# Optimization experiments

Hardware: AMD Instinct MI355X
Metric: run time of the kernel (lower is better)

Reference implementation:

```python
import jax, jax.numpy as jnp
import numpy as np

DIM = 1024
HEADS = 16
DIM_HEAD = 64
INNER = HEADS * DIM_HEAD  # 1024
EPS = 1e-5


def layer_norm(x, g, b):
    mu = jnp.mean(x, axis=-1, keepdims=True)
    var = jnp.var(x, axis=-1, keepdims=True)
    return (x - mu) * jax.lax.rsqrt(var + EPS) * g + b


def setup_inputs() -> dict:
    key = jax.random.key(0)
    ks = jax.random.split(key, 8)
    s = 0.02
    return {
        "x": jax.random.normal(ks[0], (2, 2048, DIM), dtype=jnp.float32),
        "w_qkv": jax.random.normal(ks[1], (DIM, 3 * INNER), dtype=jnp.float32) * s,
        "w_out": jax.random.normal(ks[2], (INNER, DIM), dtype=jnp.float32) * s,
        "b_out": jnp.zeros((DIM,), jnp.float32),
        "g1": jnp.ones((DIM,), jnp.float32),
        "bt1": jnp.zeros((DIM,), jnp.float32),
        "g2": jnp.ones((DIM,), jnp.float32),
        "bt2": jnp.zeros((DIM,), jnp.float32),
        "w1": jax.random.normal(ks[3], (DIM, DIM), dtype=jnp.float32) * s,  # ff hidden = dim_out = DIM
        "b1": jnp.zeros((DIM,), jnp.float32),
        "w2": jax.random.normal(ks[4], (DIM, DIM), dtype=jnp.float32) * s,
        "b2": jnp.zeros((DIM,), jnp.float32),
    }


def reference(x, w_qkv, w_out, b_out, g1, bt1, g2, bt2, w1, b1, w2, b2):
    b, n, _ = x.shape
    scale = DIM_HEAD ** (-0.5)
    x_in = x
    xl = layer_norm(x, g1, bt1)
    qkv = xl @ w_qkv  # [b, n, 3*inner]
    q, k, v = jnp.split(qkv, 3, axis=-1)
    def split_heads(t):
        return t.reshape(b, n, HEADS, DIM_HEAD).transpose(0, 2, 1, 3)  # b h n d
    q, k, v = map(split_heads, (q, k, v))
    dots = jnp.einsum('bhid,bhjd->bhij', q, k) * scale
    attn = jax.nn.softmax(dots, axis=-1)
    out = jnp.einsum('bhij,bhjd->bhid', attn, v)
    out = out.transpose(0, 2, 1, 3).reshape(b, n, INNER)
    out = out @ w_out + b_out
    out = out + x_in
    h = layer_norm(out, g2, bt2)
    h = jax.nn.gelu(h @ w1 + b1, approximate=False) @ w2 + b2
    return h + out
```

## Files before the change

kernel.cpp:

```cpp
#include <hip/hip_runtime.h>
#include <math.h>

typedef __attribute__((ext_vector_type(4))) float f32x4;
typedef __attribute__((ext_vector_type(8))) short bf16x8;
typedef __attribute__((ext_vector_type(8))) unsigned short u16x8;

#define DIM 1024
#define SEQ 2048
#define NHEADS 16
#define DH 64

__device__ __forceinline__ unsigned short f2bf(float f) {
    unsigned int u = __builtin_bit_cast(unsigned int, f);
    u += 0x7fffu + ((u >> 16) & 1u);
    return (unsigned short)(u >> 16);
}

__device__ __forceinline__ float bf2f(unsigned short s) {
    unsigned int u = (unsigned int)s << 16;
    return __builtin_bit_cast(float, u);
}

__device__ __forceinline__ unsigned int cvt_pk_bf16(float lo, float hi) {
    unsigned int r;
    asm("v_cvt_pk_bf16_f32 %0, %1, %2" : "=v"(r) : "v"(lo), "v"(hi));
    return r;
}

__device__ __forceinline__ float fexp2(float x) {
    float r;
    asm("v_exp_f32 %0, %1" : "=v"(r) : "v"(x));
    return r;
}

__device__ __forceinline__ void gld16(const unsigned short* g, unsigned short* l) {
    __builtin_amdgcn_global_load_lds((const __attribute__((address_space(1))) void*)g,
                                     (__attribute__((address_space(3))) void*)l, 16, 0, 0);
}

__global__ __launch_bounds__(256) void wtrans_ln(const float* __restrict__ wq,
                                                 const float* __restrict__ wo,
                                                 const float* __restrict__ wf1,
                                                 const float* __restrict__ wf2,
                                                 unsigned short* __restrict__ oq,
                                                 unsigned short* __restrict__ oo,
                                                 unsigned short* __restrict__ of1,
                                                 unsigned short* __restrict__ of2, float sc,
                                                 const float* __restrict__ x,
                                                 const float* __restrict__ g1,
                                                 const float* __restrict__ bt1,
                                                 unsigned short* __restrict__ xl) {
    int z = blockIdx.z;
    int bxi = blockIdx.x;
    int tid = threadIdx.x;
    if (z == 4) {
        int row = blockIdx.y * 128 + bxi;
        const float4* xr = (const float4*)(x + (size_t)row * DIM);
        float4 v = xr[tid];
        float s1 = v.x + v.y + v.z + v.w;
        float s2 = v.x * v.x + v.y * v.y + v.z * v.z + v.w * v.w;
#pragma unroll
        for (int m = 32; m >= 1; m >>= 1) {
            s1 += __shfl_xor(s1, m);
            s2 += __shfl_xor(s2, m);
        }
        __shared__ float r1[4], r2[4];
        int w = tid >> 6;
        if ((tid & 63) == 0) { r1[w] = s1; r2[w] = s2; }
        __syncthreads();
        s1 = r1[0] + r1[1] + r1[2] + r1[3];
        s2 = r2[0] + r2[1] + r2[2] + r2[3];
        float mu = s1 * (1.0f / DIM);
        float var = s2 * (1.0f / DIM) - mu * mu;
        float rstd = rsqrtf(var + 1e-5f);
        float4 g4 = ((const float4*)g1)[tid];
        float4 b4 = ((const float4*)bt1)[tid];
        ushort4 ov;
        ov.x = f2bf((v.x - mu) * rstd * g4.x + b4.x);
        ov.y = f2bf((v.y - mu) * rstd * g4.y + b4.y);
        ov.z = f2bf((v.z - mu) * rstd * g4.z + b4.z);
        ov.w = f2bf((v.w - mu) * rstd * g4.w + b4.w);
        *(ushort4*)(xl + (size_t)row * DIM + tid * 4) = ov;
        return;
    }
    if (bxi >= (z == 0 ? 96 : 32)) return;
    const float* w = z == 0 ? wq : z == 1 ? wo : z == 2 ? wf1 : wf2;
    unsigned short* wt = z == 0 ? oq : z == 1 ? oo : z == 2 ? of1 : of2;
    int N = z == 0 ? 3072 : 1024;
    int scale_n = z == 0 ? 1024 : 0;
    const int K = 1024;
    __shared__ float t[32][33];
    int n0 = bxi * 32, k0 = blockIdx.y * 32;
    int c = tid & 31, rb = tid >> 5;
#pragma unroll
    for (int i = 0; i < 4; ++i) {
        int r = rb + i * 8;
        t[r][c] = w[(size_t)(k0 + r) * N + n0 + c];
    }
    __syncthreads();
#pragma unroll
    for (int i = 0; i < 4; ++i) {
        int r = rb + i * 8;
        float v = t[c][r];
        if (n0 + r < scale_n) v *= sc;
        wt[(size_t)(n0 + r) * K + k0 + c] = f2bf(v);
    }
}

__global__ __launch_bounds__(256) void ln_bf16(const unsigned short* __restrict__ x,
                                               const float* __restrict__ g,
                                               const float* __restrict__ bt,
                                               unsigned short* __restrict__ o) {
    int row = blockIdx.x, tid = threadIdx.x;
    ushort4 v4 = *(const ushort4*)(x + (size_t)row * DIM + tid * 4);
    float vx = bf2f(v4.x), vy = bf2f(v4.y), vz = bf2f(v4.z), vw = bf2f(v4.w);
    float s1 = vx + vy + vz + vw;
    float s2 = vx * vx + vy * vy + vz * vz + vw * vw;
#pragma unroll
    for (int m = 32; m >= 1; m >>= 1) {
        s1 += __shfl_xor(s1, m);
        s2 += __shfl_xor(s2, m);
    }
    __shared__ float r1[4], r2[4];
    int w = tid >> 6;
    if ((tid & 63) == 0) { r1[w] = s1; r2[w] = s2; }
    __syncthreads();
    s1 = r1[0] + r1[1] + r1[2] + r1[3];
    s2 = r2[0] + r2[1] + r2[2] + r2[3];
    float mu = s1 * (1.0f / DIM);
    float var = s2 * (1.0f / DIM) - mu * mu;
    float rstd = rsqrtf(var + 1e-5f);
    float4 g4 = ((const float4*)g)[tid];
    float4 b4 = ((const float4*)bt)[tid];
    ushort4 ov;
    ov.x = f2bf((vx - mu) * rstd * g4.x + b4.x);
    ov.y = f2bf((vy - mu) * rstd * g4.y + b4.y);
    ov.z = f2bf((vz - mu) * rstd * g4.z + b4.z);
    ov.w = f2bf((vw - mu) * rstd * g4.w + b4.w);
    *(ushort4*)(o + (size_t)row * DIM + tid * 4) = ov;
}

template <int BN, int BK, int OBF, int BIAS, int GELU_, int RESID, int VT>
__global__ __launch_bounds__(256) void gemm_kernel(const unsigned short* __restrict__ A,
                                                   const unsigned short* __restrict__ BT,
                                                   void* __restrict__ C,
                                                   const float* __restrict__ bias,
                                                   const void* __restrict__ resid,
                                                   unsigned short* __restrict__ vt,
                                                   int M, int N, int K, int nbx) {
    constexpr int U = BK / 8;
    constexpr int NAU = 128 * U;
    constexpr int NBU = BN * U;
    constexpr int PT = (NAU + NBU) / 256;
    constexpr int NJ = BN / 32;
    constexpr int KK = BK / 32;
    extern __shared__ char smem[];
    unsigned short* As = (unsigned short*)smem;
    unsigned short* Bs = As + 3 * 128 * BK;
    int tid = threadIdx.x;
    int lane = tid & 63, w = tid >> 6;
    int l15 = lane & 15, lhi = lane >> 4;
    int nwg = gridDim.x, wg = blockIdx.x;
    int swz = (wg & 7) * (nwg >> 3) + (wg >> 3);
    int bx = swz % nbx, by = swz / nbx;
    int row0 = by * 128, col0 = bx * BN;
    int wrow = (w >> 1) * 64, wcol = (w & 1) * (16 * NJ);
    auto rh = [](int rr) -> int {
        if constexpr (U == 4) return (rr ^ (rr >> 2)) & 3;
        else return rr & (U - 1);
    };
    f32x4 zero = {0.f, 0.f, 0.f, 0.f};
    f32x4 acc[4][NJ];
#pragma unroll
    for (int i = 0; i < 4; ++i)
#pragma unroll
        for (int j = 0; j < NJ; ++j) acc[i][j] = zero;
    auto stage = [&](int buf, int kt) {
#pragma unroll
        for (int p = 0; p < PT; ++p) {
            if (p * 256 < NAU) {
                int u = tid + p * 256;
                int r = u / U, cu = u % U;
                int scu = cu ^ rh(r);
                gld16(A + (size_t)(row0 + r) * K + kt * BK + scu * 8, As + buf * 128 * BK + u * 8);
            } else {
                int ub = tid + p * 256 - NAU;
                int r = ub / U, cu = ub % U;
                int scu = cu ^ rh(r);
                gld16(BT + (size_t)(col0 + r) * K + kt * BK + scu * 8, Bs + buf * BN * BK + ub * 8);
            }
        }
    };
    int nk = K / BK;
    stage(0, 0);
    stage(1, 1);
    asm volatile("s_waitcnt vmcnt(%0)" ::"i"(PT) : "memory");
    __builtin_amdgcn_s_barrier();
    __builtin_amdgcn_sched_barrier(0);
    int cur = 0;
    for (int kt = 0; kt < nk; ++kt) {
        int nxt2 = cur + 2 >= 3 ? cur - 1 : cur + 2;
        if (kt + 2 < nk) stage(nxt2, kt + 2);
        const unsigned short* Ab = As + cur * 128 * BK;
        const unsigned short* Bb = Bs + cur * BN * BK;
        bf16x8 af[4][KK], bfr[NJ][KK];
#pragma unroll
        for (int i = 0; i < 4; ++i)
#pragma unroll
            for (int kk = 0; kk < KK; ++kk) {
                int rr = wrow + i * 16 + l15;
                int up = (kk * 4 + lhi) ^ rh(rr);
                af[i][kk] = *(const bf16x8*)&Ab[rr * BK + up * 8];
            }
#pragma unroll
        for (int j = 0; j < NJ; ++j)
#pragma unroll
            for (int kk = 0; kk < KK; ++kk) {
                int rr = wcol + j * 16 + l15;
                int up = (kk * 4 + lhi) ^ rh(rr);
                bfr[j][kk] = *(const bf16x8*)&Bb[rr * BK + up * 8];
            }
#pragma unroll
        for (int kk = 0; kk < KK; ++kk)
#pragma unroll
            for (int i = 0; i < 4; ++i)
#pragma unroll
                for (int j = 0; j < NJ; ++j)
                    acc[i][j] = __builtin_amdgcn_mfma_f32_16x16x32_bf16(af[i][kk], bfr[j][kk],
                                                                        acc[i][j], 0, 0, 0);
        __builtin_amdgcn_sched_barrier(0);
        if (kt + 1 < nk) {
            if (kt + 2 < nk)
                asm volatile("s_waitcnt vmcnt(%0)" ::"i"(PT) : "memory");
            else
                asm volatile("s_waitcnt vmcnt(0)" ::: "memory");
            __builtin_amdgcn_s_barrier();
            __builtin_amdgcn_sched_barrier(0);
        }
        cur = cur + 1 == 3 ? 0 : cur + 1;
    }
    if (VT && col0 >= 2048) {
        __syncthreads();
        unsigned short* Ct = (unsigned short*)smem;
#pragma unroll
        for (int i = 0; i < 4; ++i)
#pragma unroll
            for (int j = 0; j < NJ; ++j)
#pragma unroll
                for (int r = 0; r < 4; ++r)
                    Ct[(wrow + i * 16 + lhi * 4 + r) * 130 + (wcol + j * 16 + l15)] =
                        f2bf(acc[i][j][r]);
        __syncthreads();
        int l = tid & 63, wv = tid >> 6;
        int sig = (l & 32) | ((l & 4) << 2) | ((l & 24) >> 1) | (l & 3);
        int b = row0 >> 11, n0 = row0 & 2047;
        int h0 = (col0 - 2048) >> 6;
        for (int c = wv * 64; c < wv * 64 + 64; ++c) {
            int ntl = c & 1, hl = (c >> 1) & 1, d = c >> 2;
            unsigned short v = Ct[(ntl * 64 + sig) * 130 + hl * 64 + d];
            vt[((size_t)(b * NHEADS + h0 + hl) * DH + d) * SEQ + n0 + ntl * 64 + l] = v;
        }
        return;
    }
#pragma unroll
    for (int i = 0; i < 4; ++i)
#pragma unroll
        for (int j = 0; j < NJ; ++j)
#pragma unroll
            for (int r = 0; r < 4; ++r) {
                int row = row0 + wrow + i * 16 + lhi * 4 + r;
                int col = col0 + wcol + j * 16 + l15;
                float v = acc[i][j][r];
                if (BIAS) v += bias[col];
                if (GELU_) v = 0.5f * v * (1.0f + erff(v * 0.70710678118f));
                if (RESID == 1) v += ((const float*)resid)[(size_t)row * N + col];
                if (RESID == 2) v += bf2f(((const unsigned short*)resid)[(size_t)row * N + col]);
                if (OBF)
                    ((unsigned short*)C)[(size_t)row * N + col] = f2bf(v);
                else
                    ((float*)C)[(size_t)row * N + col] = v;
            }
}

__global__ __launch_bounds__(256) void attn_kernel(const unsigned short* __restrict__ qkv,
                                                   const unsigned short* __restrict__ vt,
                                                   unsigned short* __restrict__ o) {
    __shared__ unsigned short Ks[2][64 * 64];
    __shared__ unsigned short Vs[2][64 * 64];
    int tid = threadIdx.x;
    int lane = tid & 63, w = tid >> 6;
    int l15 = lane & 15, lhi = lane >> 4;
    int wg = blockIdx.x;
    int swz = (wg & 7) * 128 + (wg >> 3);
    int qt = swz & 31, h = (swz >> 5) & 15, b = swz >> 9;
    const unsigned short* qb =
        qkv + (size_t)(b * SEQ + qt * 64 + w * 16 + l15) * 3072 + h * DH;
    bf16x8 qf0 = *(const bf16x8*)(qb + lhi * 8);
    bf16x8 qf1 = *(const bf16x8*)(qb + 32 + lhi * 8);
    f32x4 zero = {0.f, 0.f, 0.f, 0.f};
    f32x4 oacc[4], lacc = zero;
#pragma unroll
    for (int i = 0; i < 4; ++i) oacc[i] = zero;
    const short one_s = (short)0x3F80;
    bf16x8 ones = {one_s, one_s, one_s, one_s, one_s, one_s, one_s, one_s};
    int srow = tid >> 3;
    int scx = (tid & 7) ^ (srow & 7);
    const unsigned short* kb = qkv + (size_t)b * SEQ * 3072 + 1024 + h * DH;
    const unsigned short* vb = vt + (size_t)(b * NHEADS + h) * DH * SEQ;
    const unsigned short* k0 = kb + (size_t)srow * 3072 + scx * 8;
    const unsigned short* v0 = vb + (size_t)srow * SEQ + scx * 8;
    auto stage = [&](int buf, int kt) {
        unsigned short* lk = &Ks[buf][0] + tid * 8;
        unsigned short* lv = &Vs[buf][0] + tid * 8;
        gld16(k0 + (size_t)kt * 64 * 3072, lk);
        gld16(k0 + ((size_t)kt * 64 + 32) * 3072, lk + 2048);
        gld16(v0 + kt * 64, lv);
        gld16(v0 + (size_t)32 * SEQ + kt * 64, lv + 2048);
    };
    const int NT = SEQ / 64;
    stage(0, 0);
    asm volatile("s_waitcnt vmcnt(0)" ::: "memory");
    __builtin_amdgcn_s_barrier();
    __builtin_amdgcn_sched_barrier(0);
    int kx = l15 & 7;
    for (int kt = 0; kt < NT; ++kt) {
        int cur = kt & 1;
        if (kt + 1 < NT) stage(cur ^ 1, kt + 1);
        const unsigned short* Kc = &Ks[cur][0];
        const unsigned short* Vc = &Vs[cur][0];
        f32x4 sacc[4];
#pragma unroll
        for (int nt = 0; nt < 4; ++nt) {
            bf16x8 kf0 = *(const bf16x8*)&Kc[(nt * 16 + l15) * 64 + ((lhi ^ kx) * 8)];
            bf16x8 kf1 = *(const bf16x8*)&Kc[(nt * 16 + l15) * 64 + (((4 + lhi) ^ kx) * 8)];
            f32x4 z = __builtin_amdgcn_mfma_f32_16x16x32_bf16(kf0, qf0, zero, 0, 0, 0);
            sacc[nt] = __builtin_amdgcn_mfma_f32_16x16x32_bf16(kf1, qf1, z, 0, 0, 0);
        }
        bf16x8 pf[2];
#pragma unroll
        for (int kc = 0; kc < 2; ++kc) {
            union { bf16x8 v; unsigned int u[4]; } pu;
            pu.u[0] = cvt_pk_bf16(fexp2(sacc[2 * kc][0]), fexp2(sacc[2 * kc][1]));
            pu.u[1] = cvt_pk_bf16(fexp2(sacc[2 * kc][2]), fexp2(sacc[2 * kc][3]));
            pu.u[2] = cvt_pk_bf16(fexp2(sacc[2 * kc + 1][0]), fexp2(sacc[2 * kc + 1][1]));
            pu.u[3] = cvt_pk_bf16(fexp2(sacc[2 * kc + 1][2]), fexp2(sacc[2 * kc + 1][3]));
            pf[kc] = pu.v;
        }
#pragma unroll
        for (int dt = 0; dt < 4; ++dt)
#pragma unroll
            for (int kc = 0; kc < 2; ++kc) {
                bf16x8 vf = *(const bf16x8*)&Vc[(dt * 16 + l15) * 64 + (((kc * 4 + lhi) ^ kx) * 8)];
                oacc[dt] = __builtin_amdgcn_mfma_f32_16x16x32_bf16(vf, pf[kc], oacc[dt], 0, 0, 0);
            }
        lacc = __builtin_amdgcn_mfma_f32_16x16x32_bf16(ones, pf[0], lacc, 0, 0, 0);
        lacc = __builtin_amdgcn_mfma_f32_16x16x32_bf16(ones, pf[1], lacc, 0, 0, 0);
        __builtin_amdgcn_sched_barrier(0);
        if (kt + 1 < NT) {
            asm volatile("s_waitcnt vmcnt(0)" ::: "memory");
            __builtin_amdgcn_s_barrier();
            __builtin_amdgcn_sched_barrier(0);
        }
    }
    float rl = 1.0f / lacc[0];
    size_t orow = (size_t)(b * SEQ + qt * 64 + w * 16 + l15) * DIM + h * DH;
#pragma unroll
    for (int dt = 0; dt < 4; ++dt) {
        ushort4 st;
        st.x = f2bf(oacc[dt][0] * rl);
        st.y = f2bf(oacc[dt][1] * rl);
        st.z = f2bf(oacc[dt][2] * rl);
        st.w = f2bf(oacc[dt][3] * rl);
        *(ushort4*)(o + orow + dt * 16 + lhi * 4) = st;
    }
}

extern "C" void kernel_launch(void* const* d_in, const int* in_sizes, int n_in,
                              void* d_out, int out_size, void* d_ws, size_t ws_size,
                              hipStream_t stream) {
    (void)in_sizes; (void)n_in; (void)out_size; (void)ws_size;
    const float* x = (const float*)d_in[0];
    const float* w_qkv = (const float*)d_in[1];
    const float* w_out = (const float*)d_in[2];
    const float* b_out = (const float*)d_in[3];
    const float* g1 = (const float*)d_in[4];
    const float* bt1 = (const float*)d_in[5];
    const float* g2 = (const float*)d_in[6];
    const float* bt2 = (const float*)d_in[7];
    const float* w1 = (const float*)d_in[8];
    const float* b1 = (const float*)d_in[9];
    const float* w2 = (const float*)d_in[10];
    const float* b2 = (const float*)d_in[11];
    float* out = (float*)d_out;

    char* ws = (char*)d_ws;
    size_t off = 0;
    auto alloc = [&](size_t bytes) {
        void* p = ws + off;
        off += (bytes + 255) & ~(size_t)255;
        return p;
    };
    const int R = 2 * SEQ;
    unsigned short* xl    = (unsigned short*)alloc((size_t)R * DIM * 2);
    unsigned short* wqkvT = (unsigned short*)alloc((size_t)3 * DIM * DIM * 2);
    unsigned short* woutT = (unsigned short*)alloc((size_t)DIM * DIM * 2);
    unsigned short* w1T   = (unsigned short*)alloc((size_t)DIM * DIM * 2);
    unsigned short* w2T   = (unsigned short*)alloc((size_t)DIM * DIM * 2);
    unsigned short* qkvb  = (unsigned short*)alloc((size_t)R * 3 * DIM * 2);
    unsigned short* vtb   = (unsigned short*)alloc((size_t)R * DIM * 2);
    unsigned short* attO  = (unsigned short*)alloc((size_t)R * DIM * 2);
    unsigned short* outb  = (unsigned short*)alloc((size_t)R * DIM * 2);
    unsigned short* h2    = (unsigned short*)alloc((size_t)R * DIM * 2);
    unsigned short* ffn1  = (unsigned short*)alloc((size_t)R * DIM * 2);

    const float CS = 0.125f * 1.44269504f;
    wtrans_ln<<<dim3(128, 32, 5), 256, 0, stream>>>(w_qkv, w_out, w1, w2, wqkvT, woutT, w1T, w2T,
                                                    CS, x, g1, bt1, xl);

    const unsigned int SH_QKV = (3 * 128 * 32 + 3 * 128 * 32) * 2;
    const unsigned int SH_FFN = (3 * 128 * 64 + 3 * 64 * 64) * 2;
    gemm_kernel<128, 32, 1, 0, 0, 0, 1>
        <<<dim3((3 * DIM / 128) * (R / 128)), 256, SH_QKV, stream>>>(
            xl, wqkvT, qkvb, nullptr, nullptr, vtb, R, 3 * DIM, DIM, 3 * DIM / 128);
    attn_kernel<<<2 * NHEADS * (SEQ / 64), 256, 0, stream>>>(qkvb, vtb, attO);
    gemm_kernel<64, 64, 1, 1, 0, 1, 0><<<dim3((DIM / 64) * (R / 128)), 256, SH_FFN, stream>>>(
        attO, woutT, outb, b_out, x, nullptr, R, DIM, DIM, DIM / 64);
    ln_bf16<<<R, 256, 0, stream>>>(outb, g2, bt2, h2);
    gemm_kernel<64, 64, 1, 1, 1, 0, 0><<<dim3((DIM / 64) * (R / 128)), 256, SH_FFN, stream>>>(
        h2, w1T, ffn1, b1, nullptr, nullptr, R, DIM, DIM, DIM / 64);
    gemm_kernel<64, 64, 0, 1, 0, 2, 0><<<dim3((DIM / 64) * (R / 128)), 256, SH_FFN, stream>>>(
        ffn1, w2T, out, b2, outb, nullptr, R, DIM, DIM, DIM / 64);
}
```

Before: 160.2 us.

## Use 256x256-tile QKV GEMM and move V transpose into its own kernel

Replaces the 128x128 QKV GEMM with a dedicated 512-thread kernel using 256x256 tiles, BK=64, double-buffered XOR-swizzled LDS and staged B/A prefetch interleaved with MFMA work. The goal is more operand reuse per LDS load and fewer global loads for the largest GEMM. The V transpose that used to be fused into the GEMM epilogue now runs as a separate vtrans kernel. That adds a launch and an extra read of the V slice, and the large tile grid (16x12=192 blocks) may underfill the 256 CUs.

Result: no change. 157.2 us (-1.9%).

```diff
diff --git a/kernel.cpp b/kernel.cpp
--- a/kernel.cpp
+++ b/kernel.cpp
@@ -140,13 +140,120 @@
     *(ushort4*)(o + (size_t)row * DIM + tid * 4) = ov;
 }
 
-template <int BN, int BK, int OBF, int BIAS, int GELU_, int RESID, int VT>
+__global__ __launch_bounds__(512) void gemm256_qkv(const unsigned short* __restrict__ A,
+                                                   const unsigned short* __restrict__ BT,
+                                                   unsigned short* __restrict__ C,
+                                                   int M, int N, int K, int nbx) {
+    __shared__ unsigned short As[2][256 * 64];
+    __shared__ unsigned short Bs[2][256 * 64];
+    int tid = threadIdx.x;
+    int lane = tid & 63, w = tid >> 6;
+    int l15 = lane & 15, lhi = lane >> 4;
+    int wr = w >> 2, wc = w & 3;
+    int nwg = gridDim.x, wg = blockIdx.x;
+    int swz = (wg & 7) * (nwg >> 3) + (wg >> 3);
+    int bx = swz % nbx, by = swz / nbx;
+    int row0 = by * 256, col0 = bx * 256;
+    f32x4 zero = {0.f, 0.f, 0.f, 0.f};
+    f32x4 acc[8][4];
+#pragma unroll
+    for (int i = 0; i < 8; ++i)
+#pragma unroll
+        for (int j = 0; j < 4; ++j) acc[i][j] = zero;
+    auto stageA = [&](int slot, int kt) {
+#pragma unroll
+        for (int p = 0; p < 4; ++p) {
+            int u = tid + p * 512;
+            int r = u >> 3, cu = u & 7;
+            int scu = cu ^ (r & 7);
+            gld16(A + (size_t)(row0 + r) * K + kt * 64 + scu * 8, &As[slot][0] + u * 8);
+        }
+    };
+    auto stageB = [&](int slot, int kt) {
+#pragma unroll
+        for (int p = 0; p < 4; ++p) {
+            int u = tid + p * 512;
+            int r = u >> 3, cu = u & 7;
+            int scu = cu ^ (r & 7);
+            gld16(BT + (size_t)(col0 + r) * K + kt * 64 + scu * 8, &Bs[slot][0] + u * 8);
+        }
+    };
+    int nk = K / 64;
+    stageB(0, 0);
+    stageA(0, 0);
+    stageB(1, 1);
+    stageA(1, 1);
+    asm volatile("s_waitcnt vmcnt(8)" ::: "memory");
+    __builtin_amdgcn_s_barrier();
+    __builtin_amdgcn_sched_barrier(0);
+    for (int t = 0; t < nk; ++t) {
+        int cur = t & 1;
+        const unsigned short* Ab = &As[cur][0];
+        const unsigned short* Bb = &Bs[cur][0];
+        bf16x8 bfr[4][2];
+#pragma unroll
+        for (int j = 0; j < 4; ++j)
+#pragma unroll
+            for (int kk = 0; kk < 2; ++kk) {
+                int rr = wc * 64 + j * 16 + l15;
+                bfr[j][kk] = *(const bf16x8*)&Bb[rr * 64 + (((kk * 4 + lhi) ^ (rr & 7)) * 8)];
+            }
+#pragma unroll
+        for (int q = 0; q < 4; ++q) {
+            bf16x8 af[2][2];
+#pragma unroll
+            for (int i2 = 0; i2 < 2; ++i2)
+#pragma unroll
+                for (int kk = 0; kk < 2; ++kk) {
+                    int rr = wr * 128 + (q * 2 + i2) * 16 + l15;
+                    af[i2][kk] = *(const bf16x8*)&Ab[rr * 64 + (((kk * 4 + lhi) ^ (rr & 7)) * 8)];
+                }
+#pragma unroll
+            for (int kk = 0; kk < 2; ++kk)
+#pragma unroll
+                for (int i2 = 0; i2 < 2; ++i2)
+#pragma unroll
+                    for (int j = 0; j < 4; ++j)
+                        acc[q * 2 + i2][j] = __builtin_amdgcn_mfma_f32_16x16x32_bf16(
+                            af[i2][kk], bfr[j][kk], acc[q * 2 + i2][j], 0, 0, 0);
+            if (q == 0) {
+                __builtin_amdgcn_sched_barrier(0);
+                __builtin_amdgcn_s_barrier();
+                __builtin_amdgcn_sched_barrier(0);
+                if (t + 2 < nk) stageB(cur, t + 2);
+            }
+        }
+        __builtin_amdgcn_sched_barrier(0);
+        __builtin_amdgcn_s_barrier();
+        __builtin_amdgcn_sched_barrier(0);
+        if (t + 2 < nk) stageA(cur, t + 2);
+        if (t + 1 < nk) {
+            if (t + 2 < nk)
+                asm volatile("s_waitcnt vmcnt(8)" ::: "memory");
+            else
+                asm volatile("s_waitcnt vmcnt(0)" ::: "memory");
+            __builtin_amdgcn_s_barrier();
+            __builtin_amdgcn_sched_barrier(0);
+        }
+    }
+#pragma unroll
+    for (int i = 0; i < 8; ++i)
+#pragma unroll
+        for (int j = 0; j < 4; ++j)
+#pragma unroll
+            for (int r = 0; r < 4; ++r) {
+                int row = row0 + wr * 128 + i * 16 + lhi * 4 + r;
+                int col = col0 + wc * 64 + j * 16 + l15;
+                C[(size_t)row * N + col] = f2bf(acc[i][j][r]);
+            }
+}
+
+template <int BN, int BK, int OBF, int BIAS, int GELU_, int RESID>
 __global__ __launch_bounds__(256) void gemm_kernel(const unsigned short* __restrict__ A,
                                                    const unsigned short* __restrict__ BT,
                                                    void* __restrict__ C,
                                                    const float* __restrict__ bias,
                                                    const void* __restrict__ resid,
-                                                   unsigned short* __restrict__ vt,
                                                    int M, int N, int K, int nbx) {
     constexpr int U = BK / 8;
     constexpr int NAU = 128 * U;
@@ -239,29 +346,6 @@
         }
         cur = cur + 1 == 3 ? 0 : cur + 1;
     }
-    if (VT && col0 >= 2048) {
-        __syncthreads();
-        unsigned short* Ct = (unsigned short*)smem;
-#pragma unroll
-        for (int i = 0; i < 4; ++i)
-#pragma unroll
-            for (int j = 0; j < NJ; ++j)
-#pragma unroll
-                for (int r = 0; r < 4; ++r)
-                    Ct[(wrow + i * 16 + lhi * 4 + r) * 130 + (wcol + j * 16 + l15)] =
-                        f2bf(acc[i][j][r]);
-        __syncthreads();
-        int l = tid & 63, wv = tid >> 6;
-        int sig = (l & 32) | ((l & 4) << 2) | ((l & 24) >> 1) | (l & 3);
-        int b = row0 >> 11, n0 = row0 & 2047;
-        int h0 = (col0 - 2048) >> 6;
-        for (int c = wv * 64; c < wv * 64 + 64; ++c) {
-            int ntl = c & 1, hl = (c >> 1) & 1, d = c >> 2;
-            unsigned short v = Ct[(ntl * 64 + sig) * 130 + hl * 64 + d];
-            vt[((size_t)(b * NHEADS + h0 + hl) * DH + d) * SEQ + n0 + ntl * 64 + l] = v;
-        }
-        return;
-    }
 #pragma unroll
     for (int i = 0; i < 4; ++i)
 #pragma unroll
@@ -280,6 +364,34 @@
                 else
                     ((float*)C)[(size_t)row * N + col] = v;
             }
+}
+
+__global__ __launch_bounds__(256) void vtrans_kernel(const unsigned short* __restrict__ qkv,
+                                                     unsigned short* __restrict__ vt) {
+    __shared__ unsigned short t[64 * 72];
+    int tid = threadIdx.x;
+    int nt = blockIdx.x & 31, h = (blockIdx.x >> 5) & 15, b = blockIdx.x >> 9;
+#pragma unroll
+    for (int p = 0; p < 2; ++p) {
+        int c = tid + p * 256;
+        int n = c >> 3, s = (c & 7) * 8;
+        *(uint4*)&t[n * 72 + s] =
+            *(const uint4*)(qkv + (size_t)(b * SEQ + nt * 64 + n) * 3072 + 2048 + h * 64 + s);
+    }
+    __syncthreads();
+#pragma unroll
+    for (int p = 0; p < 2; ++p) {
+        int c = tid + p * 256;
+        int d = c >> 3, s0 = (c & 7) * 8;
+        u16x8 val;
+#pragma unroll
+        for (int j = 0; j < 8; ++j) {
+            int s = s0 + j;
+            int sig = (s & 32) | ((s & 4) << 2) | ((s & 24) >> 1) | (s & 3);
+            val[j] = t[sig * 72 + d];
+        }
+        *(u16x8*)(vt + ((size_t)(b * NHEADS + h) * DH + d) * SEQ + nt * 64 + s0) = val;
+    }
 }
 
 __global__ __launch_bounds__(256) void attn_kernel(const unsigned short* __restrict__ qkv,
@@ -417,17 +529,16 @@
     wtrans_ln<<<dim3(128, 32, 5), 256, 0, stream>>>(w_qkv, w_out, w1, w2, wqkvT, woutT, w1T, w2T,
                                                     CS, x, g1, bt1, xl);
 
-    const unsigned int SH_QKV = (3 * 128 * 32 + 3 * 128 * 32) * 2;
     const unsigned int SH_FFN = (3 * 128 * 64 + 3 * 64 * 64) * 2;
-    gemm_kernel<128, 32, 1, 0, 0, 0, 1>
-        <<<dim3((3 * DIM / 128) * (R / 128)), 256, SH_QKV, stream>>>(
-            xl, wqkvT, qkvb, nullptr, nullptr, vtb, R, 3 * DIM, DIM, 3 * DIM / 128);
+    gemm256_qkv<<<dim3((R / 256) * (3 * DIM / 256)), 512, 0, stream>>>(
+        xl, wqkvT, qkvb, R, 3 * DIM, DIM, 3 * DIM / 256);
+    vtrans_kernel<<<2 * NHEADS * (SEQ / 64), 256, 0, stream>>>(qkvb, vtb);
     attn_kernel<<<2 * NHEADS * (SEQ / 64), 256, 0, stream>>>(qkvb, vtb, attO);
-    gemm_kernel<64, 64, 1, 1, 0, 1, 0><<<dim3((DIM / 64) * (R / 128)), 256, SH_FFN, stream>>>(
-        attO, woutT, outb, b_out, x, nullptr, R, DIM, DIM, DIM / 64);
+    gemm_kernel<64, 64, 1, 1, 0, 1><<<dim3((DIM / 64) * (R / 128)), 256, SH_FFN, stream>>>(
+        attO, woutT, outb, b_out, x, R, DIM, DIM, DIM / 64);
     ln_bf16<<<R, 256, 0, stream>>>(outb, g2, bt2, h2);
-    gemm_kernel<64, 64, 1, 1, 1, 0, 0><<<dim3((DIM / 64) * (R / 128)), 256, SH_FFN, stream>>>(
-        h2, w1T, ffn1, b1, nullptr, nullptr, R, DIM, DIM, DIM / 64);
-    gemm_kernel<64, 64, 0, 1, 0, 2, 0><<<dim3((DIM / 64) * (R / 128)), 256, SH_FFN, stream>>>(
-        ffn1, w2T, out, b2, outb, nullptr, R, DIM, DIM, DIM / 64);
-}
+    gemm_kernel<64, 64, 1, 1, 1, 0><<<dim3((DIM / 64) * (R / 128)), 256, SH_FFN, stream>>>(
+        h2, w1T, ffn1, b1, nullptr, R, DIM, DIM, DIM / 64);
+    gemm_kernel<64, 64, 0, 1, 0, 2><<<dim3((DIM / 64) * (R / 128)), 256, SH_FFN, stream>>>(
+        ffn1, w2T, out, b2, outb, R, DIM, DIM, DIM / 64);
+}
```
